# Performance work log

Hardware: AMD Instinct MI355X
Metric: run time of the kernel (lower is better)

The kernel has to match this reference:

```python
import jax, jax.numpy as jnp
import numpy as np

NUM_USERS = 100000
NUM_BOOKS = 50000
N_NODES = NUM_USERS + NUM_BOOKS
LATENT = 64
NUM_LAYERS = 3
N_EDGES = 2400000


def setup_inputs() -> dict:
    key = jax.random.key(0)
    ks = jax.random.split(key, 12)
    edge_index = jax.random.randint(ks[0], (2, N_EDGES), 0, N_NODES)
    embedding = jax.random.normal(ks[1], (N_NODES, LATENT), dtype=jnp.float32) * 0.1
    user_features = jax.random.normal(ks[2], (NUM_USERS, 16), dtype=jnp.float32)
    book_numerical_features = jax.random.normal(ks[3], (NUM_BOOKS, 8), dtype=jnp.float32)
    book_genre_features = jax.random.normal(ks[4], (NUM_BOOKS, 32), dtype=jnp.float32)
    W_user = jax.random.normal(ks[5], (16, LATENT), dtype=jnp.float32) * 0.1
    b_user = jnp.zeros((LATENT,), dtype=jnp.float32)
    W_num = jax.random.normal(ks[6], (8, LATENT), dtype=jnp.float32) * 0.1
    b_num = jnp.zeros((LATENT,), dtype=jnp.float32)
    W_genre = jax.random.normal(ks[7], (32, LATENT), dtype=jnp.float32) * 0.1
    b_genre = jnp.zeros((LATENT,), dtype=jnp.float32)
    return {
        "edge_index": edge_index,
        "embedding": embedding,
        "user_features": user_features,
        "book_numerical_features": book_numerical_features,
        "book_genre_features": book_genre_features,
        "W_user": W_user, "b_user": b_user,
        "W_num": W_num, "b_num": b_num,
        "W_genre": W_genre, "b_genre": b_genre,
    }


def reference(edge_index, embedding, user_features, book_numerical_features,
              book_genre_features, W_user, b_user, W_num, b_num, W_genre, b_genre):
    N = embedding.shape[0]
    # feature projections fused into initial embedding (emb0)
    user_proj = user_features @ W_user + b_user                       # [Nu, D]
    book_proj = (book_numerical_features @ W_num + b_num
                 + book_genre_features @ W_genre + b_genre)           # [Nb, D]
    emb0 = embedding + jnp.concatenate([user_proj, book_proj], axis=0)  # [N, D]

    frm, to = edge_index[0], edge_index[1]
    # symmetric degree normalization: deg counts incoming edges at target nodes
    deg = jax.ops.segment_sum(jnp.ones_like(to, dtype=emb0.dtype), to, num_segments=N)
    deg_inv_sqrt = jnp.where(deg > 0, deg ** -0.5, 0.0)
    norm = deg_inv_sqrt[frm] * deg_inv_sqrt[to]                       # [E]

    # LightGCN: gather -> scale -> scatter-add, then mean over all layer outputs
    emb = emb0
    acc = emb0
    for _ in range(NUM_LAYERS):
        msg = norm[:, None] * emb[frm]                                # [E, D]
        emb = jax.ops.segment_sum(msg, to, num_segments=N)            # [N, D]
        acc = acc + emb
    out = acc / (NUM_LAYERS + 1)
    return emb0, out
```

## Files before the change

### kernel.cpp

```cpp
#include <hip/hip_runtime.h>
#include <hip/hip_bf16.h>

typedef __hip_bfloat16 bf16;

#define D 64
#define BSH 8
#define CAP 5120
#define EPB 16384
#define PTB 1024
#define NPW 8


__global__ __launch_bounds__(256) void k_initcur(int* __restrict__ gcur, int nbk) {
    int i = blockIdx.x * 256 + threadIdx.x;
    if (i < nbk) gcur[i] = i * CAP;
}


__global__ __launch_bounds__(1024) void k_part(const int* __restrict__ frm,
                                               const int* __restrict__ to,
                                               int* __restrict__ gcur,
                                               int* __restrict__ be, int E, int nbk) {
    __shared__ int hist[1024];
    __shared__ int lofs[1024];
    __shared__ int gbase[1024];
    __shared__ int wsum[16];
    __shared__ int stage[EPB];

    int tid = threadIdx.x;
    hist[tid] = 0;
    __syncthreads();

    int base = blockIdx.x * EPB;
    int  f[16], bk[16], tl[16];
    bool va[16];
    #pragma unroll
    for (int k = 0; k < 16; k++) {
        int i = base + k * PTB + tid;
        va[k] = (i < E);
        int ic = va[k] ? i : base;
        int t = to[ic];
        f[k]  = frm[ic];
        bk[k] = t >> BSH;
        tl[k] = t & 255;
        if (va[k]) atomicAdd(&hist[bk[k]], 1);
    }
    __syncthreads();

    int c = hist[tid];
    int lane = tid & 63, wv = tid >> 6;
    int x = c;
    #pragma unroll
    for (int off = 1; off < 64; off <<= 1) {
        int y = __shfl_up(x, off);
        if (lane >= off) x += y;
    }
    if (lane == 63) wsum[wv] = x;
    __syncthreads();
    if (wv == 0) {
        int wval = (lane < 16) ? wsum[lane] : 0;
        #pragma unroll
        for (int off = 1; off < 16; off <<= 1) {
            int y = __shfl_up(wval, off);
            if (lane >= off) wval += y;
        }
        if (lane < 16) wsum[lane] = wval;
    }
    __syncthreads();
    int excl = x + (wv ? wsum[wv - 1] : 0) - c;
    lofs[tid]  = excl;
    gbase[tid] = (c > 0 && tid < nbk) ? atomicAdd(&gcur[tid], c) : 0;
    hist[tid]  = excl;
    __syncthreads();

    #pragma unroll
    for (int k = 0; k < 16; k++) {
        if (va[k]) {
            int p = atomicAdd(&hist[bk[k]], 1);
            stage[p] = (f[k] << 8) | tl[k];
        }
    }
    __syncthreads();

    for (int b = wv; b < nbk; b += 16) {
        int ls = lofs[b];
        int le = hist[b];
        int gd = gbase[b];
        for (int i = ls + lane; i < le; i += 64)
            be[gd + (i - ls)] = stage[i];
    }
}


__global__ void k_bscan(const int* __restrict__ gcur, int* __restrict__ bstart,
                        int* __restrict__ row_start, int nbk, int N, int E) {
    __shared__ int s[1024];
    int t = threadIdx.x;
    int x = (t < nbk) ? (gcur[t] - t * CAP) : 0;
    s[t] = x;
    __syncthreads();
    #pragma unroll
    for (int off = 1; off < 1024; off <<= 1) {
        int v = s[t] + ((t >= off) ? s[t - off] : 0);
        __syncthreads();
        s[t] = v;
        __syncthreads();
    }
    if (t < nbk) bstart[t] = s[t] - x;
    if (t == 0) row_start[N] = E;
}


__global__ __launch_bounds__(1024) void k_scatter(const int* __restrict__ gcur,
                                                  const int* __restrict__ bstart,
                                                  const int* __restrict__ be,
                                                  int* __restrict__ row_start,
                                                  float* __restrict__ dis,
                                                  int* __restrict__ csr, int N) {
    __shared__ int hist[256];
    __shared__ int scn[256];
    int b = blockIdx.x;
    int t = threadIdx.x;
    if (t < 256) hist[t] = 0;
    __syncthreads();

    int base = b * CAP;
    int cnt  = gcur[b] - base;
    for (int i = t; i < cnt; i += PTB)
        atomicAdd(&hist[be[base + i] & 255], 1);
    __syncthreads();

    int d = 0;
    if (t < 256) { d = hist[t]; scn[t] = d; }
    __syncthreads();
    #pragma unroll
    for (int off = 1; off < 256; off <<= 1) {
        int v = 0;
        if (t < 256) v = scn[t] + ((t >= off) ? scn[t - off] : 0);
        __syncthreads();
        if (t < 256) scn[t] = v;
        __syncthreads();
    }
    if (t < 256) {
        int rs = bstart[b] + (scn[t] - d);
        int node = (b << BSH) + t;
        if (node < N) {
            row_start[node] = rs;
            dis[node] = (d > 0) ? rsqrtf((float)d) : 0.0f;
        }
        hist[t] = rs;
    }
    __syncthreads();

    for (int i = t; i < cnt; i += PTB) {
        int rec = be[base + i];
        int pos = atomicAdd(&hist[rec & 255], 1);
        csr[pos] = rec >> 8;
    }
}


__global__ __launch_bounds__(256) void k_emb0(const float* __restrict__ emb,
                       const float* __restrict__ uf,
                       const float* __restrict__ bn,
                       const float* __restrict__ bg,
                       const float* __restrict__ Wu,
                       const float* __restrict__ bu,
                       const float* __restrict__ Wn,
                       const float* __restrict__ bnb,
                       const float* __restrict__ Wg,
                       const float* __restrict__ bgb,
                       const float* __restrict__ dis,
                       float* __restrict__ out0, bf16* __restrict__ y0,
                       int N, int NU, int ublocks) {
    int lane = threadIdx.x & 63;
    int wsub = __builtin_amdgcn_readfirstlane(threadIdx.x >> 6);

    if (blockIdx.x < ublocks) {
        float w[16];
        #pragma unroll
        for (int k = 0; k < 16; k++) w[k] = Wu[k * D + lane];
        float bias = bu[lane];

        int node0 = (blockIdx.x * 4 + wsub) * NPW;
        for (int n = 0; n < NPW; n++) {
            int node = node0 + n;
            if (node >= NU) break;
            const float4* f = (const float4*)(uf + (size_t)node * 16);
            float4 f0 = f[0], f1 = f[1], f2 = f[2], f3 = f[3];
            float p = bias
                + f0.x * w[0]  + f0.y * w[1]  + f0.z * w[2]  + f0.w * w[3]
                + f1.x * w[4]  + f1.y * w[5]  + f1.z * w[6]  + f1.w * w[7]
                + f2.x * w[8]  + f2.y * w[9]  + f2.z * w[10] + f2.w * w[11]
                + f3.x * w[12] + f3.y * w[13] + f3.z * w[14] + f3.w * w[15];
            size_t idx = (size_t)node * D + lane;
            float v = emb[idx] + p;
            out0[idx] = v;
            y0[idx]   = __float2bfloat16(dis[node] * v);
        }
    } else {
        float wn[8], wg[32];
        #pragma unroll
        for (int k = 0; k < 8; k++)  wn[k] = Wn[k * D + lane];
        #pragma unroll
        for (int k = 0; k < 32; k++) wg[k] = Wg[k * D + lane];
        float bias = bnb[lane] + bgb[lane];

        int b0 = ((blockIdx.x - ublocks) * 4 + wsub) * NPW;
        for (int n = 0; n < NPW; n++) {
            int b = b0 + n;
            int node = NU + b;
            if (node >= N) break;
            const float4* fn = (const float4*)(bn + (size_t)b * 8);
            float4 n0 = fn[0], n1 = fn[1];
            const float4* fg = (const float4*)(bg + (size_t)b * 32);
            float p = bias
                + n0.x * wn[0] + n0.y * wn[1] + n0.z * wn[2] + n0.w * wn[3]
                + n1.x * wn[4] + n1.y * wn[5] + n1.z * wn[6] + n1.w * wn[7];
            #pragma unroll
            for (int q = 0; q < 8; q++) {
                float4 g = fg[q];
                p += g.x * wg[4*q]   + g.y * wg[4*q+1]
                   + g.z * wg[4*q+2] + g.w * wg[4*q+3];
            }
            size_t idx = (size_t)node * D + lane;
            float v = emb[idx] + p;
            out0[idx] = v;
            y0[idx]   = __float2bfloat16(dis[node] * v);
        }
    }
}


static __device__ __forceinline__ unsigned int pack_bf16x2(float e, float o) {
    bf16 a = __float2bfloat16(e);
    bf16 b = __float2bfloat16(o);
    unsigned short ua = __builtin_bit_cast(unsigned short, a);
    unsigned short ub = __builtin_bit_cast(unsigned short, b);
    return (unsigned int)ua | ((unsigned int)ub << 16);
}


static __device__ __forceinline__ void gather4(
        const int* __restrict__ row_start, const int* __restrict__ csr,
        const unsigned int* __restrict__ y32, int n0, int N, int lane,
        float (&a0)[4], float (&a1)[4]) {
    int half = lane >> 5;
    int lh   = lane & 31;
    int l16  = lane & 15;

    int sv[4], ev[4];
    #pragma unroll
    for (int g = 0; g < 4; g++) {
        int node = min(n0 + g, N - 1);
        sv[g] = row_start[node];
        ev[g] = row_start[node + 1];
        a0[g] = 0.f;
        a1[g] = 0.f;
    }

    for (int c = 0; ; c++) {
        int jv[4], base[4];
        #pragma unroll
        for (int g = 0; g < 4; g++) {
            base[g] = sv[g] + 16 * c;
            jv[g] = csr[min(base[g] + l16, max(ev[g] - 1, 0))];
        }
        #pragma unroll
        for (int u = 0; u < 8; u++) {
            #pragma unroll
            for (int g = 0; g < 4; g++) {
                int idx = 2 * u + half;
                int j = __shfl(jv[g], idx);
                unsigned int d = y32[((unsigned int)j << 5) + lh];
                d = (base[g] + idx < ev[g]) ? d : 0u;
                a0[g] += __uint_as_float(d << 16);
                a1[g] += __uint_as_float(d & 0xffff0000u);
            }
        }
        bool cont = false;
        #pragma unroll
        for (int g = 0; g < 4; g++) cont = cont || (base[g] + 16 < ev[g]);
        if (!cont) break;
    }

    #pragma unroll
    for (int g = 0; g < 4; g++) {
        a0[g] += __shfl_xor(a0[g], 32);
        a1[g] += __shfl_xor(a1[g], 32);
    }
}


__global__ __launch_bounds__(256) void k_prop(const int* __restrict__ row_start,
                       const int* __restrict__ csr,
                       const float* __restrict__ dis,
                       const bf16* __restrict__ y_in,
                       bf16* __restrict__ x_out,
                       bf16* __restrict__ y_out, int N) {
    int lane = threadIdx.x & 63;
    int n0 = (blockIdx.x * 4 + (threadIdx.x >> 6)) * 4;
    if (n0 >= N) return;

    float a0[4], a1[4];
    gather4(row_start, csr, (const unsigned int*)y_in, n0, N, lane, a0, a1);

    int half = lane >> 5;
    int lh   = lane & 31;
    #pragma unroll
    for (int g = 0; g < 4; g++) {
        int node = n0 + g;
        if (node >= N) break;
        float dt = dis[node];
        float x0  = dt * a0[g];
        float x1v = dt * a1[g];
        unsigned int w = (unsigned int)node * 32 + lh;
        if (half == 0) {
            ((unsigned int*)x_out)[w] = pack_bf16x2(x0, x1v);
        } else {
            ((unsigned int*)y_out)[w] = pack_bf16x2(dt * x0, dt * x1v);
        }
    }
}


__global__ __launch_bounds__(256) void k_prop_last(const int* __restrict__ row_start,
                       const int* __restrict__ csr,
                       const float* __restrict__ dis,
                       const bf16* __restrict__ y_in,
                       const float* __restrict__ out0,
                       const bf16* __restrict__ x1,
                       const bf16* __restrict__ x2,
                       float* __restrict__ out1, int N) {
    int lane = threadIdx.x & 63;
    int n0 = (blockIdx.x * 4 + (threadIdx.x >> 6)) * 4;
    if (n0 >= N) return;

    float a0[4], a1[4];
    gather4(row_start, csr, (const unsigned int*)y_in, n0, N, lane, a0, a1);

    int half = lane >> 5;
    int lh   = lane & 31;
    #pragma unroll
    for (int g = 0; g < 4; g++) {
        int node = n0 + g;
        if (node >= N) break;
        float dt = dis[node];
        float x3e = dt * a0[g];
        float x3o = dt * a1[g];
        if (half == 0) {
            unsigned int w = (unsigned int)node * 32 + lh;
            float2 o0 = ((const float2*)out0)[w];
            unsigned int p1 = ((const unsigned int*)x1)[w];
            unsigned int p2 = ((const unsigned int*)x2)[w];
            float e1 = __uint_as_float(p1 << 16);
            float o1 = __uint_as_float(p1 & 0xffff0000u);
            float e2 = __uint_as_float(p2 << 16);
            float o2 = __uint_as_float(p2 & 0xffff0000u);
            float2 r;
            r.x = (o0.x + e1 + e2 + x3e) * 0.25f;
            r.y = (o0.y + o1 + o2 + x3o) * 0.25f;
            ((float2*)out1)[w] = r;
        }
    }
}


extern "C" void kernel_launch(void* const* d_in, const int* in_sizes, int n_in,
                              void* d_out, int out_size, void* d_ws, size_t ws_size,
                              hipStream_t stream) {
    const int E  = in_sizes[0] / 2;
    const int N  = in_sizes[1] / D;
    const int NU = in_sizes[2] / 16;
    const int nbk = (N + 255) >> BSH;

    const int*   frm = (const int*)d_in[0];
    const int*   to  = frm + E;
    const float* emb = (const float*)d_in[1];
    const float* uf  = (const float*)d_in[2];
    const float* bn  = (const float*)d_in[3];
    const float* bg  = (const float*)d_in[4];
    const float* Wu  = (const float*)d_in[5];
    const float* bu  = (const float*)d_in[6];
    const float* Wn  = (const float*)d_in[7];
    const float* bnb = (const float*)d_in[8];
    const float* Wg  = (const float*)d_in[9];
    const float* bgb = (const float*)d_in[10];

    char* p = (char*)d_ws;
    const size_t ND = (size_t)N * D;
    bf16*  y0        = (bf16*)p;   p += ND * sizeof(bf16);
    bf16*  y1        = (bf16*)p;   p += ND * sizeof(bf16);
    bf16*  x1        = (bf16*)p;   p += ND * sizeof(bf16);
    bf16*  x2        = (bf16*)p;   p += ND * sizeof(bf16);
    float* dis       = (float*)p;  p += (size_t)N * sizeof(float);
    int*   row_start = (int*)p;    p += ((size_t)N + 16) * sizeof(int);
    int*   bstart    = (int*)p;    p += 1024 * sizeof(int);
    int*   gcur      = (int*)p;    p += (size_t)nbk * sizeof(int);
    int*   csr       = (int*)p;    p += (size_t)E * sizeof(int);
    int*   be        = (int*)p;    p += (size_t)nbk * CAP * sizeof(int);

    const int TB = 256;
    const int gridProp = (N + 15) / 16;
    const int gridPart = (E + EPB - 1) / EPB;

    k_initcur<<<(nbk + TB - 1) / TB, TB, 0, stream>>>(gcur, nbk);
    k_part   <<<gridPart, PTB, 0, stream>>>(frm, to, gcur, be, E, nbk);
    k_bscan  <<<1, 1024, 0, stream>>>(gcur, bstart, row_start, nbk, N, E);
    k_scatter<<<nbk, PTB, 0, stream>>>(gcur, bstart, be, row_start, dis, csr, N);

    float* out0 = (float*)d_out;
    float* out1 = out0 + ND;

    const int NB = N - NU;
    const int uwaves  = (NU + NPW - 1) / NPW;
    const int ublocks = (uwaves + 3) / 4;
    const int bwaves  = (NB + NPW - 1) / NPW;
    const int bblocks = (bwaves + 3) / 4;
    k_emb0<<<ublocks + bblocks, TB, 0, stream>>>(emb, uf, bn, bg, Wu, bu, Wn, bnb,
                                                 Wg, bgb, dis, out0, y0, N, NU, ublocks);

    k_prop     <<<gridProp, TB, 0, stream>>>(row_start, csr, dis, y0, x1, y1, N);
    k_prop     <<<gridProp, TB, 0, stream>>>(row_start, csr, dis, y1, x2, y0, N);
    k_prop_last<<<gridProp, TB, 0, stream>>>(row_start, csr, dis, y0, out0, x1, x2, out1, N);
}
```

Before: 378.9 us.

## Process one node row per wave with 64-lane bf16 gather and uniform indices

Replaces the 4-node interleaved gather, where each half-wave loaded packed bf16 pairs and neighbour indices were broadcast by shuffles, with a simpler scheme. Each wave now handles 8 consecutive nodes one at a time. Every lane reads one bf16 element per neighbour using wave-uniform csr loads, with 8 independent accumulators. This drops the shuffles, the masking and the cross-half reduction, but each gather now moves 2-byte elements per lane instead of 4-byte pairs, and memory-level parallelism is limited to the 8 neighbours in flight for a single node.

```diff
diff --git a/kernel.cpp b/kernel.cpp
--- a/kernel.cpp
+++ b/kernel.cpp
@@ -9,6 +9,7 @@
 #define EPB 16384
 #define PTB 1024
 #define NPW 8
+#define NPWP 8
 
 
 __global__ __launch_bounds__(256) void k_initcur(int* __restrict__ gcur, int nbk) {
@@ -232,63 +233,29 @@
 }
 
 
-static __device__ __forceinline__ unsigned int pack_bf16x2(float e, float o) {
-    bf16 a = __float2bfloat16(e);
-    bf16 b = __float2bfloat16(o);
-    unsigned short ua = __builtin_bit_cast(unsigned short, a);
-    unsigned short ub = __builtin_bit_cast(unsigned short, b);
-    return (unsigned int)ua | ((unsigned int)ub << 16);
-}
-
-
-static __device__ __forceinline__ void gather4(
-        const int* __restrict__ row_start, const int* __restrict__ csr,
-        const unsigned int* __restrict__ y32, int n0, int N, int lane,
-        float (&a0)[4], float (&a1)[4]) {
-    int half = lane >> 5;
-    int lh   = lane & 31;
-    int l16  = lane & 15;
-
-    int sv[4], ev[4];
-    #pragma unroll
-    for (int g = 0; g < 4; g++) {
-        int node = min(n0 + g, N - 1);
-        sv[g] = row_start[node];
-        ev[g] = row_start[node + 1];
-        a0[g] = 0.f;
-        a1[g] = 0.f;
-    }
-
-    for (int c = 0; ; c++) {
-        int jv[4], base[4];
-        #pragma unroll
-        for (int g = 0; g < 4; g++) {
-            base[g] = sv[g] + 16 * c;
-            jv[g] = csr[min(base[g] + l16, max(ev[g] - 1, 0))];
-        }
+static __device__ __forceinline__ float gather_row(
+        const int* __restrict__ csr, const unsigned short* __restrict__ yu,
+        int s, int e, int lane) {
+    float a[8] = {0, 0, 0, 0, 0, 0, 0, 0};
+    int i = s;
+    for (; i + 8 <= e; i += 8) {
         #pragma unroll
         for (int u = 0; u < 8; u++) {
-            #pragma unroll
-            for (int g = 0; g < 4; g++) {
-                int idx = 2 * u + half;
-                int j = __shfl(jv[g], idx);
-                unsigned int d = y32[((unsigned int)j << 5) + lh];
-                d = (base[g] + idx < ev[g]) ? d : 0u;
-                a0[g] += __uint_as_float(d << 16);
-                a1[g] += __uint_as_float(d & 0xffff0000u);
-            }
-        }
-        bool cont = false;
-        #pragma unroll
-        for (int g = 0; g < 4; g++) cont = cont || (base[g] + 16 < ev[g]);
-        if (!cont) break;
-    }
-
-    #pragma unroll
-    for (int g = 0; g < 4; g++) {
-        a0[g] += __shfl_xor(a0[g], 32);
-        a1[g] += __shfl_xor(a1[g], 32);
-    }
+            int j = csr[i + u];
+            unsigned v = yu[((size_t)(unsigned)j << 6) + lane];
+            a[u] += __uint_as_float(v << 16);
+        }
+    }
+    int rem = e - i;
+    #pragma unroll
+    for (int u = 0; u < 8; u++) {
+        if (u < rem) {
+            int j = csr[i + u];
+            unsigned v = yu[((size_t)(unsigned)j << 6) + lane];
+            a[u] += __uint_as_float(v << 16);
+        }
+    }
+    return ((a[0] + a[1]) + (a[2] + a[3])) + ((a[4] + a[5]) + (a[6] + a[7]));
 }
 
 
@@ -299,27 +266,22 @@
                        bf16* __restrict__ x_out,
                        bf16* __restrict__ y_out, int N) {
     int lane = threadIdx.x & 63;
-    int n0 = (blockIdx.x * 4 + (threadIdx.x >> 6)) * 4;
-    if (n0 >= N) return;
-
-    float a0[4], a1[4];
-    gather4(row_start, csr, (const unsigned int*)y_in, n0, N, lane, a0, a1);
-
-    int half = lane >> 5;
-    int lh   = lane & 31;
-    #pragma unroll
-    for (int g = 0; g < 4; g++) {
+    int wid = __builtin_amdgcn_readfirstlane((int)(blockIdx.x * 4 + (threadIdx.x >> 6)));
+    int n0 = wid * NPWP;
+    const unsigned short* yu = (const unsigned short*)y_in;
+
+    for (int g = 0; g < NPWP; g++) {
         int node = n0 + g;
-        if (node >= N) break;
+        if (node >= N) return;
+        int s = row_start[node];
+        int e = row_start[node + 1];
+        float sum = gather_row(csr, yu, s, e, lane);
+
         float dt = dis[node];
-        float x0  = dt * a0[g];
-        float x1v = dt * a1[g];
-        unsigned int w = (unsigned int)node * 32 + lh;
-        if (half == 0) {
-            ((unsigned int*)x_out)[w] = pack_bf16x2(x0, x1v);
-        } else {
-            ((unsigned int*)y_out)[w] = pack_bf16x2(dt * x0, dt * x1v);
-        }
+        float x  = dt * sum;
+        size_t o = ((size_t)node << 6) + lane;
+        x_out[o] = __float2bfloat16(x);
+        y_out[o] = __float2bfloat16(dt * x);
     }
 }
 
@@ -333,35 +295,24 @@
                        const bf16* __restrict__ x2,
                        float* __restrict__ out1, int N) {
     int lane = threadIdx.x & 63;
-    int n0 = (blockIdx.x * 4 + (threadIdx.x >> 6)) * 4;
-    if (n0 >= N) return;
-
-    float a0[4], a1[4];
-    gather4(row_start, csr, (const unsigned int*)y_in, n0, N, lane, a0, a1);
-
-    int half = lane >> 5;
-    int lh   = lane & 31;
-    #pragma unroll
-    for (int g = 0; g < 4; g++) {
+    int wid = __builtin_amdgcn_readfirstlane((int)(blockIdx.x * 4 + (threadIdx.x >> 6)));
+    int n0 = wid * NPWP;
+    const unsigned short* yu = (const unsigned short*)y_in;
+    const unsigned short* u1 = (const unsigned short*)x1;
+    const unsigned short* u2 = (const unsigned short*)x2;
+
+    for (int g = 0; g < NPWP; g++) {
         int node = n0 + g;
-        if (node >= N) break;
-        float dt = dis[node];
-        float x3e = dt * a0[g];
-        float x3o = dt * a1[g];
-        if (half == 0) {
-            unsigned int w = (unsigned int)node * 32 + lh;
-            float2 o0 = ((const float2*)out0)[w];
-            unsigned int p1 = ((const unsigned int*)x1)[w];
-            unsigned int p2 = ((const unsigned int*)x2)[w];
-            float e1 = __uint_as_float(p1 << 16);
-            float o1 = __uint_as_float(p1 & 0xffff0000u);
-            float e2 = __uint_as_float(p2 << 16);
-            float o2 = __uint_as_float(p2 & 0xffff0000u);
-            float2 r;
-            r.x = (o0.x + e1 + e2 + x3e) * 0.25f;
-            r.y = (o0.y + o1 + o2 + x3o) * 0.25f;
-            ((float2*)out1)[w] = r;
-        }
+        if (node >= N) return;
+        int s = row_start[node];
+        int e = row_start[node + 1];
+        float sum = gather_row(csr, yu, s, e, lane);
+
+        float x3 = dis[node] * sum;
+        size_t o = ((size_t)node << 6) + lane;
+        float e1 = __uint_as_float((unsigned)u1[o] << 16);
+        float e2 = __uint_as_float((unsigned)u2[o] << 16);
+        out1[o] = (out0[o] + e1 + e2 + x3) * 0.25f;
     }
 }
 
@@ -401,7 +352,7 @@
     int*   be        = (int*)p;    p += (size_t)nbk * CAP * sizeof(int);
 
     const int TB = 256;
-    const int gridProp = (N + 15) / 16;
+    const int gridProp = (N + 4 * NPWP - 1) / (4 * NPWP);
     const int gridPart = (E + EPB - 1) / EPB;
 
     k_initcur<<<(nbk + TB - 1) / TB, TB, 0, stream>>>(gcur, nbk);
```

Result: slower. 402.4 us (+6.2%).

## Sort nodes by degree into bins and process 8 nodes per wave

Applied to the files above, without the earlier changes.

Adds a degree-binned node permutation, built during the CSR scatter plus a single-block compaction kernel. The propagation kernels then process groups of 8 similar-degree nodes per wavefront, where they used to take 4 consecutive nodes. The aim is to cut divergence: the shared chunk loop runs until the longest row in the group finishes, so grouping rows of similar length wastes fewer iterations. In exchange it adds an extra serial compaction kernel, indirect node indexing with scattered output writes, and more register pressure from the doubled group size.

```diff
diff --git a/kernel.cpp b/kernel.cpp
--- a/kernel.cpp
+++ b/kernel.cpp
@@ -9,11 +9,16 @@
 #define EPB 16384
 #define PTB 1024
 #define NPW 8
-
-
-__global__ __launch_bounds__(256) void k_initcur(int* __restrict__ gcur, int nbk) {
+#define GNP 8
+#define DBINS 64
+#define DCAP 16384
+
+
+__global__ __launch_bounds__(256) void k_initcur(int* __restrict__ gcur, int nbk,
+                                                 int* __restrict__ dgcur) {
     int i = blockIdx.x * 256 + threadIdx.x;
     if (i < nbk) gcur[i] = i * CAP;
+    if (i < DBINS) dgcur[i] = i * DCAP;
 }
 
 
@@ -116,12 +121,17 @@
                                                   const int* __restrict__ be,
                                                   int* __restrict__ row_start,
                                                   float* __restrict__ dis,
-                                                  int* __restrict__ csr, int N) {
+                                                  int* __restrict__ csr,
+                                                  int* __restrict__ dgcur,
+                                                  int* __restrict__ dperm, int N) {
     __shared__ int hist[256];
     __shared__ int scn[256];
+    __shared__ int dh[DBINS];
+    __shared__ int dbl[DBINS];
     int b = blockIdx.x;
     int t = threadIdx.x;
     if (t < 256) hist[t] = 0;
+    if (t >= 256 && t < 256 + DBINS) dh[t - 256] = 0;
     __syncthreads();
 
     int base = b * CAP;
@@ -141,21 +151,59 @@
         if (t < 256) scn[t] = v;
         __syncthreads();
     }
+    int rs = 0, node = 0, bin = 0;
+    bool vn = false;
     if (t < 256) {
-        int rs = bstart[b] + (scn[t] - d);
-        int node = (b << BSH) + t;
-        if (node < N) {
+        rs = bstart[b] + (scn[t] - d);
+        node = (b << BSH) + t;
+        vn = (node < N);
+        if (vn) {
             row_start[node] = rs;
             dis[node] = (d > 0) ? rsqrtf((float)d) : 0.0f;
-        }
-        hist[t] = rs;
-    }
+            bin = min(d, DBINS - 1);
+            atomicAdd(&dh[bin], 1);
+        }
+    }
+    __syncthreads();
+    if (t < DBINS) {
+        int c = dh[t];
+        dbl[t] = (c > 0) ? atomicAdd(&dgcur[t], c) : 0;
+        dh[t] = 0;
+    }
+    __syncthreads();
+    if (vn) {
+        int lo = atomicAdd(&dh[bin], 1);
+        dperm[dbl[bin] + lo] = node;
+    }
+    if (t < 256) hist[t] = rs;
     __syncthreads();
 
     for (int i = t; i < cnt; i += PTB) {
         int rec = be[base + i];
         int pos = atomicAdd(&hist[rec & 255], 1);
         csr[pos] = rec >> 8;
+    }
+}
+
+
+__global__ __launch_bounds__(1024) void k_dcompact(const int* __restrict__ dgcur,
+                                                   const int* __restrict__ dperm,
+                                                   int* __restrict__ perm) {
+    __shared__ int off[DBINS + 1];
+    int t = threadIdx.x;
+    if (t == 0) {
+        int acc = 0;
+        for (int b2 = 0; b2 < DBINS; b2++) {
+            off[b2] = acc;
+            acc += dgcur[b2] - b2 * DCAP;
+        }
+        off[DBINS] = acc;
+    }
+    __syncthreads();
+    for (int b2 = 0; b2 < DBINS; b2++) {
+        int o = off[b2], c = off[b2 + 1] - o;
+        for (int i = t; i < c; i += 1024)
+            perm[o + i] = dperm[b2 * DCAP + i];
     }
 }
 
@@ -241,35 +289,38 @@
 }
 
 
-static __device__ __forceinline__ void gather4(
+static __device__ __forceinline__ void gatherN(
         const int* __restrict__ row_start, const int* __restrict__ csr,
-        const unsigned int* __restrict__ y32, int n0, int N, int lane,
-        float (&a0)[4], float (&a1)[4]) {
+        const unsigned int* __restrict__ y32, const int* __restrict__ perm,
+        int n0, int N, int lane,
+        int (&nd)[GNP], float (&a0)[GNP], float (&a1)[GNP]) {
     int half = lane >> 5;
     int lh   = lane & 31;
     int l16  = lane & 15;
 
-    int sv[4], ev[4];
-    #pragma unroll
-    for (int g = 0; g < 4; g++) {
-        int node = min(n0 + g, N - 1);
+    int sv[GNP], ev[GNP];
+    #pragma unroll
+    for (int g = 0; g < GNP; g++) {
+        int slot = min(n0 + g, N - 1);
+        int node = perm[slot];
+        nd[g] = node;
         sv[g] = row_start[node];
-        ev[g] = row_start[node + 1];
+        ev[g] = (n0 + g < N) ? row_start[node + 1] : sv[g];
         a0[g] = 0.f;
         a1[g] = 0.f;
     }
 
     for (int c = 0; ; c++) {
-        int jv[4], base[4];
-        #pragma unroll
-        for (int g = 0; g < 4; g++) {
+        int jv[GNP], base[GNP];
+        #pragma unroll
+        for (int g = 0; g < GNP; g++) {
             base[g] = sv[g] + 16 * c;
             jv[g] = csr[min(base[g] + l16, max(ev[g] - 1, 0))];
         }
         #pragma unroll
         for (int u = 0; u < 8; u++) {
             #pragma unroll
-            for (int g = 0; g < 4; g++) {
+            for (int g = 0; g < GNP; g++) {
                 int idx = 2 * u + half;
                 int j = __shfl(jv[g], idx);
                 unsigned int d = y32[((unsigned int)j << 5) + lh];
@@ -280,12 +331,12 @@
         }
         bool cont = false;
         #pragma unroll
-        for (int g = 0; g < 4; g++) cont = cont || (base[g] + 16 < ev[g]);
+        for (int g = 0; g < GNP; g++) cont = cont || (base[g] + 16 < ev[g]);
         if (!cont) break;
     }
 
     #pragma unroll
-    for (int g = 0; g < 4; g++) {
+    for (int g = 0; g < GNP; g++) {
         a0[g] += __shfl_xor(a0[g], 32);
         a1[g] += __shfl_xor(a1[g], 32);
     }
@@ -297,20 +348,23 @@
                        const float* __restrict__ dis,
                        const bf16* __restrict__ y_in,
                        bf16* __restrict__ x_out,
-                       bf16* __restrict__ y_out, int N) {
+                       bf16* __restrict__ y_out,
+                       const int* __restrict__ perm, int N) {
     int lane = threadIdx.x & 63;
-    int n0 = (blockIdx.x * 4 + (threadIdx.x >> 6)) * 4;
+    int wid = __builtin_amdgcn_readfirstlane((int)(blockIdx.x * 4 + (threadIdx.x >> 6)));
+    int n0 = wid * GNP;
     if (n0 >= N) return;
 
-    float a0[4], a1[4];
-    gather4(row_start, csr, (const unsigned int*)y_in, n0, N, lane, a0, a1);
+    int nd[GNP];
+    float a0[GNP], a1[GNP];
+    gatherN(row_start, csr, (const unsigned int*)y_in, perm, n0, N, lane, nd, a0, a1);
 
     int half = lane >> 5;
     int lh   = lane & 31;
     #pragma unroll
-    for (int g = 0; g < 4; g++) {
-        int node = n0 + g;
-        if (node >= N) break;
+    for (int g = 0; g < GNP; g++) {
+        if (n0 + g >= N) break;
+        int node = nd[g];
         float dt = dis[node];
         float x0  = dt * a0[g];
         float x1v = dt * a1[g];
@@ -331,20 +385,23 @@
                        const float* __restrict__ out0,
                        const bf16* __restrict__ x1,
                        const bf16* __restrict__ x2,
-                       float* __restrict__ out1, int N) {
+                       float* __restrict__ out1,
+                       const int* __restrict__ perm, int N) {
     int lane = threadIdx.x & 63;
-    int n0 = (blockIdx.x * 4 + (threadIdx.x >> 6)) * 4;
+    int wid = __builtin_amdgcn_readfirstlane((int)(blockIdx.x * 4 + (threadIdx.x >> 6)));
+    int n0 = wid * GNP;
     if (n0 >= N) return;
 
-    float a0[4], a1[4];
-    gather4(row_start, csr, (const unsigned int*)y_in, n0, N, lane, a0, a1);
+    int nd[GNP];
+    float a0[GNP], a1[GNP];
+    gatherN(row_start, csr, (const unsigned int*)y_in, perm, n0, N, lane, nd, a0, a1);
 
     int half = lane >> 5;
     int lh   = lane & 31;
     #pragma unroll
-    for (int g = 0; g < 4; g++) {
-        int node = n0 + g;
-        if (node >= N) break;
+    for (int g = 0; g < GNP; g++) {
+        if (n0 + g >= N) break;
+        int node = nd[g];
         float dt = dis[node];
         float x3e = dt * a0[g];
         float x3o = dt * a1[g];
@@ -397,17 +454,22 @@
     int*   row_start = (int*)p;    p += ((size_t)N + 16) * sizeof(int);
     int*   bstart    = (int*)p;    p += 1024 * sizeof(int);
     int*   gcur      = (int*)p;    p += (size_t)nbk * sizeof(int);
+    int*   dgcur     = (int*)p;    p += DBINS * sizeof(int);
+    int*   perm      = (int*)p;    p += (size_t)N * sizeof(int);
     int*   csr       = (int*)p;    p += (size_t)E * sizeof(int);
     int*   be        = (int*)p;    p += (size_t)nbk * CAP * sizeof(int);
+    int*   dperm     = (int*)p;    p += (size_t)DBINS * DCAP * sizeof(int);
 
     const int TB = 256;
-    const int gridProp = (N + 15) / 16;
+    const int gridProp = (N + 4 * GNP - 1) / (4 * GNP);
     const int gridPart = (E + EPB - 1) / EPB;
 
-    k_initcur<<<(nbk + TB - 1) / TB, TB, 0, stream>>>(gcur, nbk);
+    k_initcur<<<(nbk + TB - 1) / TB, TB, 0, stream>>>(gcur, nbk, dgcur);
     k_part   <<<gridPart, PTB, 0, stream>>>(frm, to, gcur, be, E, nbk);
     k_bscan  <<<1, 1024, 0, stream>>>(gcur, bstart, row_start, nbk, N, E);
-    k_scatter<<<nbk, PTB, 0, stream>>>(gcur, bstart, be, row_start, dis, csr, N);
+    k_scatter<<<nbk, PTB, 0, stream>>>(gcur, bstart, be, row_start, dis, csr,
+                                       dgcur, dperm, N);
+    k_dcompact<<<1, 1024, 0, stream>>>(dgcur, dperm, perm);
 
     float* out0 = (float*)d_out;
     float* out1 = out0 + ND;
@@ -420,7 +482,8 @@
     k_emb0<<<ublocks + bblocks, TB, 0, stream>>>(emb, uf, bn, bg, Wu, bu, Wn, bnb,
                                                  Wg, bgb, dis, out0, y0, N, NU, ublocks);
 
-    k_prop     <<<gridProp, TB, 0, stream>>>(row_start, csr, dis, y0, x1, y1, N);
-    k_prop     <<<gridProp, TB, 0, stream>>>(row_start, csr, dis, y1, x2, y0, N);
-    k_prop_last<<<gridProp, TB, 0, stream>>>(row_start, csr, dis, y0, out0, x1, x2, out1, N);
-}
+    k_prop     <<<gridProp, TB, 0, stream>>>(row_start, csr, dis, y0, x1, y1, perm, N);
+    k_prop     <<<gridProp, TB, 0, stream>>>(row_start, csr, dis, y1, x2, y0, perm, N);
+    k_prop_last<<<gridProp, TB, 0, stream>>>(row_start, csr, dis, y0, out0, x1, x2,
+                                             out1, perm, N);
+}
```

After: 512.8 us. +35.4%, slower.
